# Kernel tuning notes

Measured on AMD Instinct MI355X. Metric: run time of the kernel, lower is better.

Reference implementation:

```python
import jax, jax.numpy as jnp
import numpy as np

D_MODEL = 512
NUM_HEADS = 8
D_K = D_MODEL // NUM_HEADS
SCALE = 1.0 / np.sqrt(D_K).astype(np.float32)


def _relative_shift(x):
    # x: (B, H, S, P) pos scores from Q @ P^T; Transformer-XL shift trick.
    b, h, s, p = x.shape
    x = jnp.pad(x, ((0, 0), (0, 0), (0, 0), (1, 0)))   # (B,H,S,P+1)
    x = x.reshape(b, h, p + 1, s)[:, :, 1:, :]          # drop first row
    x = x.reshape(b, h, s, p)[:, :, :, :s]
    return x


def setup_inputs() -> dict:
    key = jax.random.key(0)
    ks = jax.random.split(key, 10)
    B, S = 4, 2048
    glorot = lambda k: jax.random.uniform(
        k, (D_MODEL, D_MODEL), jnp.float32,
        -np.sqrt(6.0 / (2 * D_MODEL)), np.sqrt(6.0 / (2 * D_MODEL)))
    return {
        "inputs": jax.random.normal(ks[0], (B, S, D_MODEL), jnp.float32),
        "pos_enc": jax.random.normal(ks[1], (1, S, D_MODEL), jnp.float32),
        "W_q": glorot(ks[2]),
        "W_k": glorot(ks[3]),
        "W_v": glorot(ks[4]),
        "W_o": glorot(ks[5]),
        "W_pos": glorot(ks[6]),
        "u_bias": jnp.zeros((NUM_HEADS, D_K), jnp.float32),
        "v_bias": jnp.zeros((NUM_HEADS, D_K), jnp.float32),
    }


def reference(inputs, pos_enc, W_q, W_k, W_v, W_o, W_pos, u_bias, v_bias):
    B, S, _ = inputs.shape
    split = lambda x, b: x.reshape(b, S, NUM_HEADS, D_K).transpose(0, 2, 1, 3)
    Q = split(inputs @ W_q, B)        # (B,H,S,dk)
    K = split(inputs @ W_k, B)
    V = split(inputs @ W_v, B)
    P = split(pos_enc @ W_pos, 1)      # (1,H,S,dk)
    u = u_bias[None, :, None, :]
    v = v_bias[None, :, None, :]
    content_score = jnp.einsum('bhid,bhjd->bhij', Q + u, K)
    pos_score = jnp.einsum('bhid,xhjd->bhij', Q + v, P)  # broadcast over batch
    pos_score = _relative_shift(pos_score)
    scores = (content_score + pos_score) * SCALE
    attn = jax.nn.softmax(scores, axis=-1)  # no dropout (inference)
    context = jnp.einsum('bhij,bhjd->bhid', attn, V)
    context = context.transpose(0, 2, 1, 3).reshape(B, S, D_MODEL)
    return context @ W_o
```

## Files before the change

### kernel.cpp

```cpp
#include <hip/hip_runtime.h>
#include <hip/hip_bf16.h>
#include <math.h>

#define SEQ 2048
#define NH 8
#define DK 64
#define DM 512
#define QSCALE 0.18033688011112042f
#define PPAD (SEQ + 128)
#define POFF 64
#define KSTR 72
#define PSTR 36
#define ASTR 34

typedef unsigned short ushortT;
typedef short s16x8 __attribute__((ext_vector_type(8)));
typedef float f32x4 __attribute__((ext_vector_type(4)));

#define MFMA16 __builtin_amdgcn_mfma_f32_16x16x32_bf16

static __device__ __forceinline__ ushortT f2bf(float x) {
  __hip_bfloat16 h = __float2bfloat16(x);
  ushortT u;
  __builtin_memcpy(&u, &h, 2);
  return u;
}

static __device__ __forceinline__ float fexp2(float x) {
  return __builtin_amdgcn_exp2f(x);
}

static __device__ __forceinline__ s16x8 pack8(const float* p) {
  ushortT u[8];
#pragma unroll
  for (int i = 0; i < 8; ++i) u[i] = f2bf(p[i]);
  s16x8 out;
  __builtin_memcpy(&out, u, 16);
  return out;
}

static __device__ __forceinline__ int pinv(int j) {
  return (j < 16) ? ((j >> 2) * 8 + (j & 3)) : (((j >> 2) - 4) * 8 + 4 + (j & 3));
}

__global__ __launch_bounds__(256)
void cast_in(const float* __restrict__ X, const float* __restrict__ PE,
             ushortT* __restrict__ Xb, ushortT* __restrict__ PEb) {
  const size_t i4 = (size_t)blockIdx.x * 256 + threadIdx.x;
  const size_t NX = (size_t)4 * SEQ * DM / 4;
  const float4 v = (i4 < NX) ? *(const float4*)(X + i4 * 4)
                             : *(const float4*)(PE + (i4 - NX) * 4);
  ushortT o[4] = {f2bf(v.x), f2bf(v.y), f2bf(v.z), f2bf(v.w)};
  ushortT* dst = (i4 < NX) ? (Xb + i4 * 4) : (PEb + (i4 - NX) * 4);
  *(ulonglong1*)dst = *(ulonglong1*)o;
}

__global__ __launch_bounds__(256)
void transpose_w(const float* __restrict__ w0, const float* __restrict__ w1,
                 const float* __restrict__ w2, const float* __restrict__ w3,
                 const float* __restrict__ w4, ushortT* __restrict__ out) {
  __shared__ float ts[32][33];
  const int z = blockIdx.z;
  const float* w = (z == 0) ? w0 : (z == 1) ? w1 : (z == 2) ? w2 : (z == 3) ? w3 : w4;
  ushortT* o = out + (size_t)z * DM * DM;
  const int k0 = blockIdx.x * 32, n0 = blockIdx.y * 32;
  const int tx = threadIdx.x, ty = threadIdx.y;
#pragma unroll
  for (int i = 0; i < 4; ++i)
    ts[ty + i * 8][tx] = w[(size_t)(k0 + ty + i * 8) * DM + n0 + tx];
  __syncthreads();
#pragma unroll
  for (int i = 0; i < 4; ++i)
    o[(size_t)(n0 + ty + i * 8) * DM + k0 + tx] = f2bf(ts[tx][ty + i * 8]);
}

__global__ __launch_bounds__(256)
void gemm_mfma(const ushortT* __restrict__ A, const ushortT* __restrict__ Bt,
               const float* __restrict__ ubv, const float* __restrict__ vbv,
               ushortT* __restrict__ qu, ushortT* __restrict__ qv,
               ushortT* __restrict__ kb, ushortT* __restrict__ vt,
               float* __restrict__ of, int mode) {
  __shared__ ushortT As[128][ASTR];
  __shared__ ushortT Bs[128][ASTR];
  const int tid = threadIdx.x;
  const int w = tid >> 6, lane = tid & 63;
  const int c = lane & 15, q = lane >> 4;
  const int wm = w >> 1, wn = w & 1;
  const int m0 = blockIdx.x * 128, n0 = blockIdx.y * 128;
  const int lr = tid >> 1, lh = (tid & 1) * 16;

  f32x4 acc[4][4];
#pragma unroll
  for (int mt = 0; mt < 4; ++mt)
#pragma unroll
    for (int nt = 0; nt < 4; ++nt) acc[mt][nt] = (f32x4){0.f, 0.f, 0.f, 0.f};

  const ushortT* Ar = A + (size_t)(m0 + lr) * DM + lh;
  const ushortT* Br = Bt + (size_t)(n0 + lr) * DM + lh;
  uint4 a0 = *(const uint4*)(Ar);
  uint4 a1 = *(const uint4*)(Ar + 8);
  uint4 b0 = *(const uint4*)(Br);
  uint4 b1 = *(const uint4*)(Br + 8);

  for (int k0 = 0; k0 < DM; k0 += 32) {
    __syncthreads();
    *(uint4*)&As[lr][lh] = a0; *(uint4*)&As[lr][lh + 8] = a1;
    *(uint4*)&Bs[lr][lh] = b0; *(uint4*)&Bs[lr][lh + 8] = b1;
    __syncthreads();
    if (k0 + 32 < DM) {
      a0 = *(const uint4*)(Ar + k0 + 32);
      a1 = *(const uint4*)(Ar + k0 + 40);
      b0 = *(const uint4*)(Br + k0 + 32);
      b1 = *(const uint4*)(Br + k0 + 40);
    }
    s16x8 af[4], bf[4];
#pragma unroll
    for (int mt = 0; mt < 4; ++mt)
      af[mt] = *(const s16x8*)&As[wm * 64 + mt * 16 + c][q * 8];
#pragma unroll
    for (int nt = 0; nt < 4; ++nt)
      bf[nt] = *(const s16x8*)&Bs[wn * 64 + nt * 16 + c][q * 8];
#pragma unroll
    for (int mt = 0; mt < 4; ++mt)
#pragma unroll
      for (int nt = 0; nt < 4; ++nt)
        acc[mt][nt] = MFMA16(af[mt], bf[nt], acc[mt][nt], 0, 0, 0);
  }

#pragma unroll
  for (int mt = 0; mt < 4; ++mt)
#pragma unroll
    for (int nt = 0; nt < 4; ++nt)
#pragma unroll
      for (int r = 0; r < 4; ++r) {
        const int gm = m0 + wm * 64 + mt * 16 + q * 4 + r;
        const int gn = n0 + wn * 64 + nt * 16 + c;
        const float v = acc[mt][nt][r];
        const int bb = gm >> 11, s = gm & (SEQ - 1);
        if (mode == 0) {
          const int z = gn >> 9, gn5 = gn & 511;
          const int h = gn5 >> 6, d = gn5 & 63;
          if (z == 0) {
            const size_t base = (((size_t)bb * NH + h) * SEQ + s) * DK + d;
            qu[base] = f2bf((v + ubv[gn5]) * QSCALE);
            qv[base] = f2bf((v + vbv[gn5]) * QSCALE);
          } else if (z == 1) {
            kb[(((size_t)bb * NH + h) * SEQ + s) * DK + d] = f2bf(v);
          } else {
            const int s_il = (s & ~31) | pinv(s & 31);
            vt[(((size_t)bb * NH + h) * DK + d) * SEQ + s_il] = f2bf(v);
          }
        } else if (mode == 3) {
          const int h = gn >> 6, d = gn & 63;
          qu[((size_t)h * PPAD + POFF + gm) * DK + d] = f2bf(v);
        } else {
          of[(size_t)gm * DM + gn] = v;
        }
      }
}

static __device__ __forceinline__ f32x4 band_gemm(const ushortT* pb, int tile,
                                                  int c, int q, s16x8 a0, s16x8 a1) {
  const ushortT* pc = pb + (ptrdiff_t)(tile * 16 + c) * DK + q * 8;
  f32x4 G = {0.f, 0.f, 0.f, 0.f};
  G = MFMA16(a0, *(const s16x8*)pc, G, 0, 0, 0);
  G = MFMA16(a1, *(const s16x8*)(pc + 32), G, 0, 0, 0);
  return G;
}

static __device__ __forceinline__ void write_band(float (*E)[PSTR], int c, int m_w,
                                                  f32x4 b0, f32x4 b1, f32x4 b2) {
  const f32x4 bb[3] = {b0, b1, b2};
#pragma unroll
  for (int t = 0; t < 3; ++t)
#pragma unroll
    for (int r = 0; r < 4; ++r) {
      const int kcol = t * 16 + c + (m_w + r) - 15;
      if (kcol >= 0 && kcol < 32) E[m_w + r][pinv(kcol)] = bb[t][r];
    }
}

__global__ __launch_bounds__(256, 3)
void attn_mfma(const ushortT* __restrict__ Qu, const ushortT* __restrict__ Qv,
               const ushortT* __restrict__ Kb, const ushortT* __restrict__ Vt,
               const ushortT* __restrict__ Pp, ushortT* __restrict__ ctxb) {
  const int n = blockIdx.x;
  const int xcd = n & 7, idx = n >> 3;
  const int b = idx >> 5, iblk = idx & 31;
  const int h = xcd, bh = b * 8 + h;
  const int tid = threadIdx.x;
  const int w = tid >> 6, lane = tid & 63;
  const int c = lane & 15, q = lane >> 4;
  const int i0 = iblk * 64;
  const int iw = i0 + w * 16;

  __shared__ ushortT Ks[64][KSTR];
  __shared__ ushortT Vs[64][KSTR];
  __shared__ float E1[4][2][16][PSTR];
  __shared__ float E2[4][16][PSTR];
  __shared__ float Lb[4][16];

  const ushortT* Qub = Qu + ((size_t)bh * SEQ + iw) * DK;
  const ushortT* Qvb = Qv + ((size_t)bh * SEQ + iw) * DK;
  const ushortT* Kbh = Kb + (size_t)bh * SEQ * DK;
  const ushortT* Vbh = Vt + (size_t)bh * DK * SEQ;
  const ushortT* Ph  = Pp + ((size_t)h * PPAD + POFF) * DK;

  const s16x8 qu0 = *(const s16x8*)(Qub + (size_t)c * DK + q * 8);
  const s16x8 qu1 = *(const s16x8*)(Qub + (size_t)c * DK + 32 + q * 8);
  const s16x8 qv0 = *(const s16x8*)(Qvb + (size_t)c * DK + q * 8);
  const s16x8 qv1 = *(const s16x8*)(Qvb + (size_t)c * DK + 32 + q * 8);
  const s16x8 qw0 = *(const s16x8*)(Qvb + (size_t)(c + 1) * DK + q * 8);
  const s16x8 qw1 = *(const s16x8*)(Qvb + (size_t)(c + 1) * DK + 32 + q * 8);

  int joff[8];
#pragma unroll
  for (int jj = 0; jj < 8; ++jj)
    joff[jj] = (jj < 4) ? (4 * q + jj) : (16 + 4 * q + (jj - 4));

  f32x4 O[4];
#pragma unroll
  for (int r = 0; r < 4; ++r) O[r] = (f32x4){0.f, 0.f, 0.f, 0.f};
  float lrow = 0.f;
  f32x4 e2c = (f32x4){0.f, 0.f, 0.f, 0.f};
  bool hv1 = false, hv2 = false;
  const int jt = iw & ~31;
  const int m_w = q * 4;

  {
    const ushortT* gk = Kbh;
    uint4 k0v = *(const uint4*)(gk + tid * 8);
    uint4 k1v = *(const uint4*)(gk + 2048 + tid * 8);
    const ushortT* gv = Vbh + (size_t)(tid >> 2) * SEQ + (tid & 3) * 16;
    uint4 v0v = *(const uint4*)gv;
    uint4 v1v = *(const uint4*)(gv + 8);
    *(uint4*)&Ks[tid >> 3][(tid & 7) * 8] = k0v;
    *(uint4*)&Ks[32 + (tid >> 3)][(tid & 7) * 8] = k1v;
    *(uint4*)&Vs[tid >> 2][(tid & 3) * 16] = v0v;
    *(uint4*)&Vs[tid >> 2][(tid & 3) * 16 + 8] = v1v;
  }
  __syncthreads();

  if (jt > 0) {
    const ushortT* pb1 = Ph + (ptrdiff_t)(0 - iw + SEQ - 16) * DK;
    f32x4 b0 = band_gemm(pb1, 0, c, q, qv0, qv1);
    f32x4 b1 = band_gemm(pb1, 1, c, q, qv0, qv1);
    e2c = band_gemm(pb1, 2, c, q, qv0, qv1);
    hv1 = true;
    write_band(E1[w][0], c, m_w, b0, b1, e2c);
  }

#define PV_FROM(pr, jl)                                                       \
  {                                                                           \
    lrow += pr[0] + pr[1] + pr[2] + pr[3] + pr[4] + pr[5] + pr[6] + pr[7];    \
    const s16x8 pa = pack8(pr);                                               \
    _Pragma("unroll")                                                         \
    for (int dt = 0; dt < 4; ++dt) {                                          \
      const s16x8 vb = *(const s16x8*)&Vs[dt * 16 + c][(jl) + q * 8];         \
      O[dt] = MFMA16(pa, vb, O[dt], 0, 0, 0);                                 \
    }                                                                         \
  }

  for (int ch = 0; ch < 32; ++ch) {
    const bool more = (ch + 1) < 32;
    uint4 k0v, k1v, v0v, v1v;
    if (more) {
      const ushortT* gk = Kbh + (size_t)(ch + 1) * 64 * DK;
      k0v = *(const uint4*)(gk + tid * 8);
      k1v = *(const uint4*)(gk + 2048 + tid * 8);
      const ushortT* gv = Vbh + (size_t)(tid >> 2) * SEQ + (ch + 1) * 64 + (tid & 3) * 16;
      v0v = *(const uint4*)gv;
      v1v = *(const uint4*)(gv + 8);
    }
#pragma unroll
    for (int t = 0; t < 2; ++t) {
      const int nn = ch * 2 + t;
      const int j0 = nn * 32;
      const int jl = t * 32;
      const int drel = j0 - iw;
      const bool curB = (j0 >= jt) && (j0 < jt + 64);

      f32x4 S0 = {0.f, 0.f, 0.f, 0.f}, S1 = {0.f, 0.f, 0.f, 0.f};
      {
        const ushortT* ka = &Ks[jl + c][q * 8];
        S0 = MFMA16(*(const s16x8*)ka, qu0, S0, 0, 0, 0);
        S0 = MFMA16(*(const s16x8*)(ka + 32), qu1, S0, 0, 0, 0);
        const ushortT* ka2 = &Ks[jl + 16 + c][q * 8];
        S1 = MFMA16(*(const s16x8*)ka2, qu0, S1, 0, 0, 0);
        S1 = MFMA16(*(const s16x8*)(ka2 + 32), qu1, S1, 0, 0, 0);
      }

      if (curB) {
        {
          const ushortT* pb1 = Ph + (ptrdiff_t)(drel + SEQ - 16) * DK;
          f32x4 b0 = band_gemm(pb1, 0, c, q, qv0, qv1);
          f32x4 b1 = band_gemm(pb1, 1, c, q, qv0, qv1);
          f32x4 b2 = band_gemm(pb1, 2, c, q, qv0, qv1);
          write_band(E1[w][nn & 1], c, m_w, b0, b1, b2);
        }
        {
          const ushortT* pb2 = Ph + (ptrdiff_t)(drel - 17) * DK;
          f32x4 b0 = band_gemm(pb2, 0, c, q, qw0, qw1);
          f32x4 b1 = band_gemm(pb2, 1, c, q, qw0, qw1);
          f32x4 b2 = band_gemm(pb2, 2, c, q, qw0, qw1);
          write_band(E2[w], c, m_w, b0, b1, b2);
        }
        const float* e1r = &E1[w][nn & 1][c][q * 8];
        const float* e2r = &E2[w][c][q * 8];
        float4 aA = *(const float4*)e1r, aB = *(const float4*)(e1r + 4);
        float4 bA = *(const float4*)e2r, bB = *(const float4*)(e2r + 4);
        float f1[8] = {aA.x, aA.y, aA.z, aA.w, aB.x, aB.y, aB.z, aB.w};
        float f2[8] = {bA.x, bA.y, bA.z, bA.w, bB.x, bB.y, bB.z, bB.w};
        float sv[8] = {S0[0], S0[1], S0[2], S0[3], S1[0], S1[1], S1[2], S1[3]};
        float pr[8];
#pragma unroll
        for (int jj = 0; jj < 8; ++jj) {
          const int dlt = drel + joff[jj] - c;
          const float g = (dlt <= 0) ? f1[jj] : ((dlt == 1) ? 0.0f : f2[jj]);
          pr[jj] = fexp2(sv[jj] + g);
        }
        PV_FROM(pr, jl)
      } else {
        const float* e1r = &E1[w][nn & 1][c][q * 8];
        float4 fA = *(const float4*)e1r, fB = *(const float4*)(e1r + 4);
        float pr[8] = {fexp2(S0[0] + fA.x), fexp2(S0[1] + fA.y),
                       fexp2(S0[2] + fA.z), fexp2(S0[3] + fA.w),
                       fexp2(S1[0] + fB.x), fexp2(S1[1] + fB.y),
                       fexp2(S1[2] + fB.z), fexp2(S1[3] + fB.w)};
        PV_FROM(pr, jl)
      }

      if (nn + 1 < 64) {
        const int j0n = j0 + 32;
        const bool nxtB = (j0n >= jt) && (j0n < jt + 64);
        if (!nxtB) {
          const int dreln = j0n - iw;
          if (j0n < jt) {
            const ushortT* pb1 = Ph + (ptrdiff_t)(dreln + SEQ - 16) * DK;
            f32x4 b0;
            if (hv1) b0 = e2c;
            else { b0 = band_gemm(pb1, 0, c, q, qv0, qv1); hv1 = true; }
            f32x4 b1 = band_gemm(pb1, 1, c, q, qv0, qv1);
            e2c = band_gemm(pb1, 2, c, q, qv0, qv1);
            write_band(E1[w][(nn + 1) & 1], c, m_w, b0, b1, e2c);
          } else {
            const ushortT* pb2 = Ph + (ptrdiff_t)(dreln - 17) * DK;
            f32x4 b0;
            if (hv2) b0 = e2c;
            else { b0 = band_gemm(pb2, 0, c, q, qw0, qw1); hv2 = true; }
            f32x4 b1 = band_gemm(pb2, 1, c, q, qw0, qw1);
            e2c = band_gemm(pb2, 2, c, q, qw0, qw1);
            write_band(E1[w][(nn + 1) & 1], c, m_w, b0, b1, e2c);
          }
        }
      }
    }
    __syncthreads();
    if (more) {
      *(uint4*)&Ks[tid >> 3][(tid & 7) * 8] = k0v;
      *(uint4*)&Ks[32 + (tid >> 3)][(tid & 7) * 8] = k1v;
      *(uint4*)&Vs[tid >> 2][(tid & 3) * 16] = v0v;
      *(uint4*)&Vs[tid >> 2][(tid & 3) * 16 + 8] = v1v;
    }
    __syncthreads();
  }

  lrow += __shfl_xor(lrow, 16);
  lrow += __shfl_xor(lrow, 32);
  if (q == 0) Lb[w][c] = lrow;
  float inv[4];
#pragma unroll
  for (int r = 0; r < 4; ++r) inv[r] = 1.0f / Lb[w][q * 4 + r];
#pragma unroll
  for (int dt = 0; dt < 4; ++dt)
#pragma unroll
    for (int r = 0; r < 4; ++r) {
      const int i = iw + q * 4 + r;
      ctxb[((size_t)b * SEQ + i) * DM + h * DK + dt * 16 + c] = f2bf(O[dt][r] * inv[r]);
    }
}

extern "C" void kernel_launch(void* const* d_in, const int* in_sizes, int n_in,
                              void* d_out, int out_size, void* d_ws, size_t ws_size,
                              hipStream_t stream) {
  (void)in_sizes; (void)n_in; (void)out_size; (void)ws_size;
  const float* X   = (const float*)d_in[0];
  const float* PE  = (const float*)d_in[1];
  const float* Wq  = (const float*)d_in[2];
  const float* Wk  = (const float*)d_in[3];
  const float* Wv  = (const float*)d_in[4];
  const float* Wo  = (const float*)d_in[5];
  const float* Wp  = (const float*)d_in[6];
  const float* ubv = (const float*)d_in[7];
  const float* vbv = (const float*)d_in[8];

  const size_t NX = (size_t)4 * SEQ * DM;
  const size_t NP = (size_t)SEQ * DM;
  const size_t NW = (size_t)DM * DM;
  ushortT* Xb  = (ushortT*)d_ws;
  ushortT* PEb = Xb + NX;
  ushortT* Wt  = PEb + NP;
  ushortT* qu  = Wt + 5 * NW;
  ushortT* qv  = qu + NX;
  ushortT* kb  = qv + NX;
  ushortT* vt  = kb + NX;
  ushortT* pp  = vt + NX;
  ushortT* ctx = pp + (size_t)NH * PPAD * DK;
  float* outp = (float*)d_out;

  hipLaunchKernelGGL(cast_in, dim3((NX + NP) / 4 / 256), dim3(256), 0, stream, X, PE, Xb, PEb);
  hipLaunchKernelGGL(transpose_w, dim3(16, 16, 5), dim3(32, 8), 0, stream, Wq, Wk, Wv, Wp, Wo, Wt);
  dim3 blk(256);
  hipLaunchKernelGGL(gemm_mfma, dim3(64, 12), blk, 0, stream, Xb, Wt, ubv, vbv,
                     qu, qv, kb, vt, (float*)nullptr, 0);
  hipLaunchKernelGGL(gemm_mfma, dim3(16, 4), blk, 0, stream, PEb, Wt + 3 * NW, ubv, vbv,
                     pp, (ushortT*)nullptr, (ushortT*)nullptr, (ushortT*)nullptr, (float*)nullptr, 3);
  hipLaunchKernelGGL(attn_mfma, dim3(1024), blk, 0, stream, qu, qv, kb, vt, pp, ctx);
  hipLaunchKernelGGL(gemm_mfma, dim3(64, 4), blk, 0, stream, ctx, Wt + 4 * NW, ubv, vbv,
                     (ushortT*)nullptr, (ushortT*)nullptr, (ushortT*)nullptr, (ushortT*)nullptr, outp, 4);
}
```

Before: 358.6 us.

## Prefetch next band P tiles early, simplify band writes, drop E2, raise occupancy

```diff
diff --git a/kernel.cpp b/kernel.cpp
--- a/kernel.cpp
+++ b/kernel.cpp
@@ -168,19 +168,29 @@
   return G;
 }
 
-static __device__ __forceinline__ void write_band(float (*E)[PSTR], int c, int m_w,
-                                                  f32x4 b0, f32x4 b1, f32x4 b2) {
-  const f32x4 bb[3] = {b0, b1, b2};
-#pragma unroll
-  for (int t = 0; t < 3; ++t)
-#pragma unroll
-    for (int r = 0; r < 4; ++r) {
-      const int kcol = t * 16 + c + (m_w + r) - 15;
-      if (kcol >= 0 && kcol < 32) E[m_w + r][pinv(kcol)] = bb[t][r];
-    }
-}
-
-__global__ __launch_bounds__(256, 3)
+static __device__ __forceinline__ f32x4 band_gemm_r(s16x8 a0, s16x8 a1,
+                                                    s16x8 p0, s16x8 p1) {
+  f32x4 G = {0.f, 0.f, 0.f, 0.f};
+  G = MFMA16(a0, p0, G, 0, 0, 0);
+  G = MFMA16(a1, p1, G, 0, 0, 0);
+  return G;
+}
+
+static __device__ __forceinline__ void write_band2(float (*E)[PSTR], int c, int m_w,
+                                                   f32x4 b0, f32x4 b1, f32x4 b2) {
+#pragma unroll
+  for (int r = 0; r < 4; ++r) {
+    const int v = c + m_w + r - 15;
+    const bool lo = (v >= 0);
+    const int j1 = lo ? v : v + 16;
+    const int p = ((j1 >> 2) << 3) | (j1 & 3);
+    float* row = &E[m_w + r][p];
+    row[0] = lo ? b0[r] : b1[r];
+    row[4] = lo ? b1[r] : b2[r];
+  }
+}
+
+__global__ __launch_bounds__(256, 4)
 void attn_mfma(const ushortT* __restrict__ Qu, const ushortT* __restrict__ Qv,
                const ushortT* __restrict__ Kb, const ushortT* __restrict__ Vt,
                const ushortT* __restrict__ Pp, ushortT* __restrict__ ctxb) {
@@ -197,7 +207,6 @@
   __shared__ ushortT Ks[64][KSTR];
   __shared__ ushortT Vs[64][KSTR];
   __shared__ float E1[4][2][16][PSTR];
-  __shared__ float E2[4][16][PSTR];
   __shared__ float Lb[4][16];
 
   const ushortT* Qub = Qu + ((size_t)bh * SEQ + iw) * DK;
@@ -247,7 +256,7 @@
     f32x4 b1 = band_gemm(pb1, 1, c, q, qv0, qv1);
     e2c = band_gemm(pb1, 2, c, q, qv0, qv1);
     hv1 = true;
-    write_band(E1[w][0], c, m_w, b0, b1, e2c);
+    write_band2(E1[w][0], c, m_w, b0, b1, e2c);
   }
 
 #define PV_FROM(pr, jl)                                                       \
@@ -279,6 +288,31 @@
       const int jl = t * 32;
       const int drel = j0 - iw;
       const bool curB = (j0 >= jt) && (j0 < jt + 64);
+      const int j0n = j0 + 32;
+      const bool nxtB = (j0n >= jt) && (j0n < jt + 64);
+      const bool haveNext = (nn + 1 < 64) && !nxtB;
+      const bool nextA = (j0n < jt);
+
+      s16x8 p10, p11, p20, p21;
+      const ushortT* pbn = nullptr;
+      if (haveNext) {
+        const int dreln = j0n - iw;
+        pbn = nextA ? (Ph + (ptrdiff_t)(dreln + SEQ - 16) * DK)
+                    : (Ph + (ptrdiff_t)(dreln - 17) * DK);
+        const ushortT* pc1 = pbn + (ptrdiff_t)(16 + c) * DK + q * 8;
+        const ushortT* pc2 = pbn + (ptrdiff_t)(32 + c) * DK + q * 8;
+        p10 = *(const s16x8*)pc1;
+        p11 = *(const s16x8*)(pc1 + 32);
+        p20 = *(const s16x8*)pc2;
+        p21 = *(const s16x8*)(pc2 + 32);
+      }
+
+      float4 fA, fB;
+      if (!curB) {
+        const float* e1r = &E1[w][nn & 1][c][q * 8];
+        fA = *(const float4*)e1r;
+        fB = *(const float4*)(e1r + 4);
+      }
 
       f32x4 S0 = {0.f, 0.f, 0.f, 0.f}, S1 = {0.f, 0.f, 0.f, 0.f};
       {
@@ -296,17 +330,17 @@
           f32x4 b0 = band_gemm(pb1, 0, c, q, qv0, qv1);
           f32x4 b1 = band_gemm(pb1, 1, c, q, qv0, qv1);
           f32x4 b2 = band_gemm(pb1, 2, c, q, qv0, qv1);
-          write_band(E1[w][nn & 1], c, m_w, b0, b1, b2);
+          write_band2(E1[w][nn & 1], c, m_w, b0, b1, b2);
         }
         {
           const ushortT* pb2 = Ph + (ptrdiff_t)(drel - 17) * DK;
           f32x4 b0 = band_gemm(pb2, 0, c, q, qw0, qw1);
           f32x4 b1 = band_gemm(pb2, 1, c, q, qw0, qw1);
           f32x4 b2 = band_gemm(pb2, 2, c, q, qw0, qw1);
-          write_band(E2[w], c, m_w, b0, b1, b2);
+          write_band2(E1[w][(nn + 1) & 1], c, m_w, b0, b1, b2);
         }
         const float* e1r = &E1[w][nn & 1][c][q * 8];
-        const float* e2r = &E2[w][c][q * 8];
+        const float* e2r = &E1[w][(nn + 1) & 1][c][q * 8];
         float4 aA = *(const float4*)e1r, aB = *(const float4*)(e1r + 4);
         float4 bA = *(const float4*)e2r, bB = *(const float4*)(e2r + 4);
         float f1[8] = {aA.x, aA.y, aA.z, aA.w, aB.x, aB.y, aB.z, aB.w};
@@ -321,8 +355,6 @@
         }
         PV_FROM(pr, jl)
       } else {
-        const float* e1r = &E1[w][nn & 1][c][q * 8];
-        float4 fA = *(const float4*)e1r, fB = *(const float4*)(e1r + 4);
         float pr[8] = {fexp2(S0[0] + fA.x), fexp2(S0[1] + fA.y),
                        fexp2(S0[2] + fA.z), fexp2(S0[3] + fA.w),
                        fexp2(S1[0] + fB.x), fexp2(S1[1] + fB.y),
@@ -330,29 +362,21 @@
         PV_FROM(pr, jl)
       }
 
-      if (nn + 1 < 64) {
-        const int j0n = j0 + 32;
-        const bool nxtB = (j0n >= jt) && (j0n < jt + 64);
-        if (!nxtB) {
-          const int dreln = j0n - iw;
-          if (j0n < jt) {
-            const ushortT* pb1 = Ph + (ptrdiff_t)(dreln + SEQ - 16) * DK;
-            f32x4 b0;
-            if (hv1) b0 = e2c;
-            else { b0 = band_gemm(pb1, 0, c, q, qv0, qv1); hv1 = true; }
-            f32x4 b1 = band_gemm(pb1, 1, c, q, qv0, qv1);
-            e2c = band_gemm(pb1, 2, c, q, qv0, qv1);
-            write_band(E1[w][(nn + 1) & 1], c, m_w, b0, b1, e2c);
-          } else {
-            const ushortT* pb2 = Ph + (ptrdiff_t)(dreln - 17) * DK;
-            f32x4 b0;
-            if (hv2) b0 = e2c;
-            else { b0 = band_gemm(pb2, 0, c, q, qw0, qw1); hv2 = true; }
-            f32x4 b1 = band_gemm(pb2, 1, c, q, qw0, qw1);
-            e2c = band_gemm(pb2, 2, c, q, qw0, qw1);
-            write_band(E1[w][(nn + 1) & 1], c, m_w, b0, b1, e2c);
-          }
+      if (haveNext) {
+        f32x4 b0, b1, b2;
+        if (nextA) {
+          if (hv1) b0 = e2c;
+          else { b0 = band_gemm(pbn, 0, c, q, qv0, qv1); hv1 = true; }
+          b1 = band_gemm_r(qv0, qv1, p10, p11);
+          b2 = band_gemm_r(qv0, qv1, p20, p21);
+        } else {
+          if (hv2) b0 = e2c;
+          else { b0 = band_gemm(pbn, 0, c, q, qw0, qw1); hv2 = true; }
+          b1 = band_gemm_r(qw0, qw1, p10, p11);
+          b2 = band_gemm_r(qw0, qw1, p20, p21);
         }
+        e2c = b2;
+        write_band2(E1[w][(nn + 1) & 1], c, m_w, b0, b1, b2);
       }
     }
     __syncthreads();
```

Measured after the change: 474.1 us. +32.2%, slower.
